# Optimization experiments

Measured on AMD Instinct MI355X. Metric: run time of the kernel, lower is better.

The kernel has to match this reference:

```python
import jax, jax.numpy as jnp
import numpy as np
import math

D_MODEL = 1024
NUM_HEADS = 16
D_HEAD = D_MODEL // NUM_HEADS          # 64
N_FREQ = D_HEAD // 2 + 1               # 33 rfft bins
COMPRESSION_RATIO = 0.5


def setup_inputs() -> dict:
    key = jax.random.key(0)
    k_x, k_qkv, k_out, k_b, k_m = jax.random.split(key, 5)
    B, S = 2, 2048
    x = jax.random.normal(k_x, (B, S, D_MODEL), dtype=jnp.float32)
    # Linear weights stored as [in, out] (torch Linear uses [out, in]; math identical).
    w_qkv = jax.random.normal(k_qkv, (D_MODEL, 3 * D_MODEL), dtype=jnp.float32) / math.sqrt(D_MODEL)
    w_out = jax.random.normal(k_out, (D_MODEL, D_MODEL), dtype=jnp.float32) / math.sqrt(D_MODEL)
    b_out = jax.random.normal(k_b, (D_MODEL,), dtype=jnp.float32) * 0.01
    # Learned per-frequency-bin mask logits of AdaptiveFrequencyMask(d_state=d_head).
    # Initialized around logit(compression_ratio) with small noise.
    init_logit = math.log(COMPRESSION_RATIO / (1.0 - COMPRESSION_RATIO))
    mask_logits = init_logit + 0.1 * jax.random.normal(k_m, (N_FREQ,), dtype=jnp.float32)
    return {"x": x, "w_qkv": w_qkv, "w_out": w_out, "b_out": b_out, "mask_logits": mask_logits}


def _spectral_filter(t, mask):
    # rfft over d_head dim, apply learned soft mask, inverse rfft.  t: [B,H,S,dh]
    tf = jnp.fft.rfft(t, axis=-1)          # [B,H,S,N_FREQ] complex
    tf = tf * mask                          # broadcast real mask over bins
    return jnp.fft.irfft(tf, n=t.shape[-1], axis=-1).astype(t.dtype)


def reference(x, w_qkv, w_out, b_out, mask_logits):
    B, S, D = x.shape
    H, dh = NUM_HEADS, D_HEAD
    qkv = x @ w_qkv                                         # [B,S,3D]
    q, k, v = jnp.split(qkv, 3, axis=-1)
    # [B,S,D] -> [B,H,S,dh]
    to_heads = lambda t: t.reshape(B, S, H, dh).transpose(0, 2, 1, 3)
    q, k, v = to_heads(q), to_heads(k), to_heads(v)
    mask = jax.nn.sigmoid(mask_logits)                      # [N_FREQ]
    q = _spectral_filter(q, mask)
    k = _spectral_filter(k, mask)
    scores = jnp.einsum('bhqd,bhkd->bhqk', q, k) / math.sqrt(dh)
    attn = jax.nn.softmax(scores, axis=-1)                  # dropout p=0 (eval)
    out = jnp.einsum('bhqk,bhkd->bhqd', attn, v)
    out = out.transpose(0, 2, 1, 3).reshape(B, S, D)
    return out @ w_out + b_out
```

## Files before the change

kernel.cpp:

```cpp
#include <hip/hip_runtime.h>

#define S_LEN 2048
#define NH    16
#define DH    64
#define DM    1024
#define NQKV  3072

typedef __attribute__((ext_vector_type(8))) __bf16 bf16x8;
typedef __attribute__((ext_vector_type(4))) float  f32x4;
typedef unsigned short ushort_t;

static __device__ __forceinline__ unsigned short bf16b(float f) {
  return __builtin_bit_cast(unsigned short, (__bf16)f);
}

static __device__ __forceinline__ float exp2v(float x) {
  return __builtin_amdgcn_exp2f(x);
}

static __device__ __forceinline__ bf16x8 pack8(float4 f0, float4 f1) {
  uint4 v;
  v.x = ((unsigned)bf16b(f0.y) << 16) | bf16b(f0.x);
  v.y = ((unsigned)bf16b(f0.w) << 16) | bf16b(f0.z);
  v.z = ((unsigned)bf16b(f1.y) << 16) | bf16b(f1.x);
  v.w = ((unsigned)bf16b(f1.w) << 16) | bf16b(f1.z);
  return __builtin_bit_cast(bf16x8, v);
}

static __device__ __forceinline__ void glds16(const void* g, void* l) {
  __builtin_amdgcn_global_load_lds((const __attribute__((address_space(1))) unsigned int*)g,
                                   (__attribute__((address_space(3))) unsigned int*)l, 16, 0, 0);
}

#define OFF_WT  65536ull
#define OFF_WOT 6356992ull
#define OFF_Q   8454144ull
#define OFF_K   16842752ull
#define OFF_V   25231360ull
#define OFF_AO  33619968ull

__global__ __launch_bounds__(256) void k_prep(const float* __restrict__ wqkv,
                                              const float* __restrict__ wout,
                                              const float* __restrict__ x,
                                              const float* __restrict__ logits,
                                              unsigned short* __restrict__ Wt,
                                              unsigned short* __restrict__ Wot,
                                              unsigned short* __restrict__ xb) {
  __shared__ __align__(16) char sbuf[16640];
  int bid = blockIdx.x;
  int t = threadIdx.x;

  if (bid < 256) {
    float* msk = (float*)sbuf;
    float* Kd  = (float*)(sbuf + 144);
    ushort_t (*Fb)[72] = (ushort_t(*)[72])(sbuf + 416);
    if (t < 33) msk[t] = 1.0f / (1.0f + __expf(-logits[t]));
    __syncthreads();
    if (t < 64) {
      float acc = msk[0];
      #pragma unroll
      for (int f = 1; f < 32; ++f) {
        int r = (f * t) & 63;
        acc += 2.0f * msk[f] * __cosf((float)r * (6.28318530717958647692f / 64.0f));
      }
      acc += msk[32] * ((t & 1) ? -1.0f : 1.0f);
      Kd[t] = acc * (1.0f / 64.0f);
    }
    __syncthreads();
    for (int idx = t; idx < 4096; idx += 256) {
      int j = idx >> 6, i = idx & 63;
      Fb[j][i] = bf16b(Kd[(j - i) & 63]);
    }
    __syncthreads();

    int lane = t & 63, w = t >> 6;
    int m16 = lane & 15, quad = lane >> 4;
    int kx = bid >> 5, yy = bid & 31;
    int which = yy >> 4, h = yy & 15;
    int base = which * 1024 + h * 64;

    bf16x8 af0 = *(const bf16x8*)(&Fb[w * 16 + m16][quad * 8]);
    bf16x8 af1 = *(const bf16x8*)(&Fb[w * 16 + m16][32 + quad * 8]);

    f32x4 acc[8] = {};
    #pragma unroll 2
    for (int n = 0; n < 8; ++n) {
      const float* Wg = wqkv + (size_t)(kx * 128 + n * 16 + m16) * NQKV + base + quad * 8;
      float4 a0 = *(const float4*)(Wg);
      float4 a1 = *(const float4*)(Wg + 4);
      float4 b0 = *(const float4*)(Wg + 32);
      float4 b1 = *(const float4*)(Wg + 36);
      acc[n] = __builtin_amdgcn_mfma_f32_16x16x32_bf16(af0, pack8(a0, a1), acc[n], 0, 0, 0);
      acc[n] = __builtin_amdgcn_mfma_f32_16x16x32_bf16(af1, pack8(b0, b1), acc[n], 0, 0, 0);
    }
    float sc = (which == 0) ? 0.18033688011112042f : 1.0f;
    #pragma unroll
    for (int n = 0; n < 8; ++n) {
      #pragma unroll
      for (int r = 0; r < 4; ++r) {
        int j = w * 16 + quad * 4 + r;
        Wt[(size_t)(base + j) * DM + kx * 128 + n * 16 + m16] = bf16b(acc[n][r] * sc);
      }
    }
  } else if (bid < 768) {
    float (*Ts)[65] = (float(*)[65])sbuf;
    int b1 = bid - 256;
    if (b1 < 256) {
      int kt = b1 & 15, nt = b1 >> 4;
      int cb = 2048 + nt * 64, kbase = kt * 64;
      #pragma unroll
      for (int p = 0; p < 16; ++p) {
        int kk = p * 4 + (t >> 6);
        Ts[kk][t & 63] = wqkv[(size_t)(kbase + kk) * NQKV + cb + (t & 63)];
      }
      __syncthreads();
      #pragma unroll
      for (int p = 0; p < 16; ++p) {
        int nn = p * 4 + (t >> 6);
        Wt[(size_t)(cb + nn) * DM + kbase + (t & 63)] = bf16b(Ts[t & 63][nn]);
      }
    } else {
      int b2 = b1 - 256;
      int kt = b2 & 15, nt = b2 >> 4;
      int cb = nt * 64, kbase = kt * 64;
      #pragma unroll
      for (int p = 0; p < 16; ++p) {
        int kk = p * 4 + (t >> 6);
        Ts[kk][t & 63] = wout[(size_t)(kbase + kk) * DM + cb + (t & 63)];
      }
      __syncthreads();
      #pragma unroll
      for (int p = 0; p < 16; ++p) {
        int nn = p * 4 + (t >> 6);
        Wot[(size_t)(cb + nn) * DM + kbase + (t & 63)] = bf16b(Ts[t & 63][nn]);
      }
    }
  } else {
    size_t i = ((size_t)(bid - 768) * 256 + t) * 8;
    const float4* xp = (const float4*)(x + i);
    float4 a = xp[0], b = xp[1];
    uint4 v;
    v.x = ((unsigned)bf16b(a.y) << 16) | bf16b(a.x);
    v.y = ((unsigned)bf16b(a.w) << 16) | bf16b(a.z);
    v.z = ((unsigned)bf16b(b.y) << 16) | bf16b(b.x);
    v.w = ((unsigned)bf16b(b.w) << 16) | bf16b(b.z);
    *(uint4*)(xb + i) = v;
  }
}

__device__ __forceinline__ void gemm_core_async(const unsigned short* __restrict__ A,
                                                const unsigned short* __restrict__ Bw,
                                                int bm, int bn, unsigned short* smem,
                                                f32x4 (&acc)[4][4]) {
  unsigned short* As = smem;
  unsigned short* Bs = smem + 8192;
  int t = threadIdx.x, lane = t & 63, w = t >> 6;
  int m16 = lane & 15, quad = lane >> 4;
  int wr = (w >> 1) * 64, wc = (w & 1) * 64;
  int lr = lane >> 3, lc = lane & 7;
  int gc = lc ^ lr;
  int xr = m16 & 7;
  const unsigned short* Agb = A  + (size_t)(bm * 128) * DM + gc * 8;
  const unsigned short* Bgb = Bw + (size_t)(bn * 128) * DM + gc * 8;

  for (int k0 = 0; k0 < DM; k0 += 64) {
    #pragma unroll
    for (int p = 0; p < 4; ++p) {
      int row = p * 32 + w * 8 + lr;
      glds16(Agb + (size_t)row * DM + k0, As + row * 64 + lc * 8);
      glds16(Bgb + (size_t)row * DM + k0, Bs + row * 64 + lc * 8);
    }
    __syncthreads();
    #pragma unroll
    for (int kk = 0; kk < 2; ++kk) {
      bf16x8 af[4], bfr[4];
      #pragma unroll
      for (int i = 0; i < 4; ++i)
        af[i] = *(const bf16x8*)(As + (wr + i * 16 + m16) * 64 + ((kk * 4 + quad) ^ xr) * 8);
      #pragma unroll
      for (int j = 0; j < 4; ++j)
        bfr[j] = *(const bf16x8*)(Bs + (wc + j * 16 + m16) * 64 + ((kk * 4 + quad) ^ xr) * 8);
      #pragma unroll
      for (int i = 0; i < 4; ++i)
        #pragma unroll
        for (int j = 0; j < 4; ++j)
          acc[i][j] = __builtin_amdgcn_mfma_f32_16x16x32_bf16(af[i], bfr[j], acc[i][j], 0, 0, 0);
    }
    __syncthreads();
  }
}

__global__ __launch_bounds__(256) void k_gemm_qkv(const unsigned short* __restrict__ xb,
                                                  const unsigned short* __restrict__ Bw,
                                                  unsigned short* __restrict__ Qb,
                                                  unsigned short* __restrict__ Kb,
                                                  unsigned short* __restrict__ Vt) {
  __shared__ __align__(16) unsigned short smem[18432];
  f32x4 acc[4][4] = {};
  int bn = blockIdx.x, bm = blockIdx.y;
  gemm_core_async(xb, Bw, bm, bn, smem, acc);

  int t = threadIdx.x, lane = t & 63, w = t >> 6;
  int m16 = lane & 15, quad = lane >> 4;
  int wr = (w >> 1) * 64, wc = (w & 1) * 64;
  int b = bm >> 4, srow = (bm & 15) * 128;
  int which = bn >> 3;
  ushort_t (*Tr)[130] = (ushort_t(*)[130])smem;
  if (which < 2) {
    #pragma unroll
    for (int i = 0; i < 4; ++i)
      #pragma unroll
      for (int j = 0; j < 4; ++j)
        #pragma unroll
        for (int r = 0; r < 4; ++r)
          Tr[wr + i * 16 + quad * 4 + r][wc + j * 16 + m16] = bf16b(acc[i][j][r]);
    __syncthreads();
    int row = t >> 1, half = t & 1;
    int cloc = bn * 128 + half * 64 - which * 1024;
    int h = cloc >> 6;
    unsigned short* dst = (which ? Kb : Qb) +
        ((size_t)(b * 16 + h) * 2048 + srow + row) * 64;
    #pragma unroll
    for (int p = 0; p < 8; ++p)
      *(uint4*)(dst + p * 8) = *(const uint4*)(&Tr[row][half * 64 + p * 8]);
  } else {
    #pragma unroll
    for (int i = 0; i < 4; ++i)
      #pragma unroll
      for (int j = 0; j < 4; ++j)
        #pragma unroll
        for (int r = 0; r < 4; ++r)
          Tr[wc + j * 16 + m16][wr + i * 16 + quad * 4 + r] = bf16b(acc[i][j][r]);
    __syncthreads();
    int dl = t >> 1, half = t & 1;
    int cloc = (bn - 16) * 128 + dl;
    int h = cloc >> 6, d = cloc & 63;
    unsigned short* dst = Vt + ((size_t)(b * 16 + h) * 64 + d) * 2048 + srow + half * 64;
    #pragma unroll
    for (int p = 0; p < 8; ++p)
      *(uint4*)(dst + p * 8) = *(const uint4*)(&Tr[dl][half * 64 + p * 8]);
  }
}

__global__ __launch_bounds__(512, 4) void k_attn(const unsigned short* __restrict__ Qb,
                                                 const unsigned short* __restrict__ Kb,
                                                 const unsigned short* __restrict__ Vt,
                                                 unsigned short* __restrict__ AO) {
  __shared__ __align__(16) unsigned short smem[25088];
  int t = threadIdx.x;
  int w = t >> 6, lane = t & 63;
  int m16 = lane & 15, quad = lane >> 4;
  int bid = blockIdx.x;
  int jj = bid >> 3;
  int bh = ((jj & 3) << 3) + (bid & 7);
  int qbase = (jj >> 2) * 128 + w * 16;

  const unsigned short* Qp = Qb + ((size_t)bh * S_LEN + qbase + m16) * DH + quad * 8;
  bf16x8 aq0 = *(const bf16x8*)(Qp);
  bf16x8 aq1 = *(const bf16x8*)(Qp + 32);
  const unsigned short* Kbase = Kb + (size_t)bh * S_LEN * DH;
  const unsigned short* Vbase = Vt + (size_t)bh * DH * S_LEN;

  unsigned short* Pw = smem + 16384 + w * 1088;
  int xr = m16 & 7;

  int trow = t >> 3;
  int tcol = t & 7;
  int gswz = tcol ^ (trow & 7);

  f32x4 o[4] = {};
  float l = 0.f;
  f32x4 zero = {0.f, 0.f, 0.f, 0.f};

  glds16(Kbase + (size_t)trow * 64 + gswz * 8,    smem + trow * 64 + tcol * 8);
  glds16(Vbase + (size_t)trow * S_LEN + gswz * 8, smem + 8192 + trow * 64 + tcol * 8);
  __syncthreads();

  #pragma unroll 1
  for (int kt = 0; kt < S_LEN / 64; ++kt) {
    int cur = kt & 1, nxt = cur ^ 1;
    if (kt + 1 < S_LEN / 64) {
      int kk = (kt + 1) * 64;
      glds16(Kbase + (size_t)(kk + trow) * 64 + gswz * 8,
             smem + nxt * 4096 + trow * 64 + tcol * 8);
      glds16(Vbase + (size_t)trow * S_LEN + kk + gswz * 8,
             smem + 8192 + nxt * 4096 + trow * 64 + tcol * 8);
    }
    unsigned short* Ksh = smem + cur * 4096;
    unsigned short* Vsh = smem + 8192 + cur * 4096;

    f32x4 st[4];
    #pragma unroll
    for (int g = 0; g < 4; ++g) {
      int rk = g * 16 + m16;
      bf16x8 kf0 = *(const bf16x8*)(Ksh + rk * 64 + ((quad ^ xr) * 8));
      bf16x8 kf1 = *(const bf16x8*)(Ksh + rk * 64 + (((4 + quad) ^ xr) * 8));
      st[g] = __builtin_amdgcn_mfma_f32_16x16x32_bf16(kf0, aq0, zero, 0, 0, 0);
      st[g] = __builtin_amdgcn_mfma_f32_16x16x32_bf16(kf1, aq1, st[g], 0, 0, 0);
    }
    #pragma unroll
    for (int g = 0; g < 4; ++g) {
      float p0 = exp2v(st[g][0]), p1 = exp2v(st[g][1]);
      float p2 = exp2v(st[g][2]), p3 = exp2v(st[g][3]);
      l += (p0 + p1) + (p2 + p3);
      uint2 pk;
      pk.x = ((unsigned)bf16b(p1) << 16) | bf16b(p0);
      pk.y = ((unsigned)bf16b(p3) << 16) | bf16b(p2);
      *(uint2*)(Pw + m16 * 68 + g * 16 + quad * 4) = pk;
    }
    #pragma unroll
    for (int c = 0; c < 2; ++c) {
      bf16x8 ap = *(const bf16x8*)(Pw + m16 * 68 + c * 32 + quad * 8);
      #pragma unroll
      for (int j = 0; j < 4; ++j) {
        int dv = j * 16 + m16;
        bf16x8 bv = *(const bf16x8*)(Vsh + dv * 64 + (((c * 4 + quad) ^ xr) * 8));
        o[j] = __builtin_amdgcn_mfma_f32_16x16x32_bf16(ap, bv, o[j], 0, 0, 0);
      }
    }
    __syncthreads();
  }

  l += __shfl_xor(l, 16); l += __shfl_xor(l, 32);
  float iv = 1.0f / l;
  int b = bh >> 4, h = bh & 15;
  #pragma unroll
  for (int r = 0; r < 4; ++r) {
    float v0 = __shfl(iv, quad * 4 + r);
    size_t row0 = (size_t)b * S_LEN + qbase + quad * 4 + r;
    unsigned short* d0 = AO + row0 * DM + h * DH + m16;
    #pragma unroll
    for (int j = 0; j < 4; ++j)
      d0[j * 16] = bf16b(o[j][r] * v0);
  }
}

__global__ __launch_bounds__(256) void k_gemm_out(const unsigned short* __restrict__ A,
                                                  const unsigned short* __restrict__ Bw,
                                                  const float* __restrict__ bias,
                                                  float* __restrict__ out) {
  __shared__ __align__(16) unsigned short smem[18432];
  f32x4 acc[4][4] = {};
  int bn = blockIdx.x, bm = blockIdx.y;
  gemm_core_async(A, Bw, bm, bn, smem, acc);

  int t = threadIdx.x, lane = t & 63, w = t >> 6;
  int m16 = lane & 15, quad = lane >> 4;
  int wr = (w >> 1) * 64, wc = (w & 1) * 64;
  #pragma unroll
  for (int i = 0; i < 4; ++i) {
    int grow = bm * 128 + wr + i * 16 + quad * 4;
    #pragma unroll
    for (int j = 0; j < 4; ++j) {
      int gc = bn * 128 + wc + j * 16 + m16;
      float bb = bias[gc];
      #pragma unroll
      for (int r = 0; r < 4; ++r)
        out[(size_t)(grow + r) * DM + gc] = acc[i][j][r] + bb;
    }
  }
}

extern "C" void kernel_launch(void* const* d_in, const int* in_sizes, int n_in,
                              void* d_out, int out_size, void* d_ws, size_t ws_size,
                              hipStream_t stream) {
  const float* x    = (const float*)d_in[0];
  const float* wqkv = (const float*)d_in[1];
  const float* wout = (const float*)d_in[2];
  const float* bout = (const float*)d_in[3];
  const float* mlog = (const float*)d_in[4];
  char* ws = (char*)d_ws;
  unsigned short* Wt  = (unsigned short*)(ws + OFF_WT);
  unsigned short* Wot = (unsigned short*)(ws + OFF_WOT);
  unsigned short* Qb  = (unsigned short*)(ws + OFF_Q);
  unsigned short* Kb  = (unsigned short*)(ws + OFF_K);
  unsigned short* Vt  = (unsigned short*)(ws + OFF_V);
  unsigned short* xb  = (unsigned short*)(ws + OFF_AO);
  unsigned short* AO  = (unsigned short*)(ws + OFF_AO);
  float* out = (float*)d_out;

  k_prep<<<dim3(2816), dim3(256), 0, stream>>>(wqkv, wout, x, mlog, Wt, Wot, xb);
  k_gemm_qkv<<<dim3(24, 32), dim3(256), 0, stream>>>(xb, Wt, Qb, Kb, Vt);
  k_attn<<<dim3(512), dim3(512), 0, stream>>>(Qb, Kb, Vt, AO);
  k_gemm_out<<<dim3(8, 32), dim3(256), 0, stream>>>(AO, Wot, bout, out);
}
```

Baseline: 215.8 us.

## Split attention over two key halves with atomic fp32 accumulation and normalize pass

Splits each head's key range into two halves so the attention grid doubles to 1024 blocks of 256 threads. Each wave now processes 32 query rows, and V is read straight from global memory into registers instead of being staged through LDS. Unnormalized partial outputs and row sums are combined with atomicAdd into zeroed fp32 buffers, and a new k_norm kernel divides and converts to bf16. This is meant to raise parallelism and reuse of each K fragment, at the cost of two memsets, many global atomics and an extra pass over a 16 MB buffer.

```diff
diff --git a/kernel.cpp b/kernel.cpp
--- a/kernel.cpp
+++ b/kernel.cpp
@@ -33,6 +33,7 @@
 }
 
 #define OFF_WT  65536ull
+#define OFF_LB  65536ull
 #define OFF_WOT 6356992ull
 #define OFF_Q   8454144ull
 #define OFF_K   16842752ull
@@ -242,97 +243,146 @@
   }
 }
 
-__global__ __launch_bounds__(512, 4) void k_attn(const unsigned short* __restrict__ Qb,
+__global__ __launch_bounds__(256, 4) void k_attn(const unsigned short* __restrict__ Qb,
                                                  const unsigned short* __restrict__ Kb,
                                                  const unsigned short* __restrict__ Vt,
-                                                 unsigned short* __restrict__ AO) {
-  __shared__ __align__(16) unsigned short smem[25088];
+                                                 float* __restrict__ dout,
+                                                 float* __restrict__ l_buf) {
+  __shared__ __align__(16) unsigned short smem[16896];
   int t = threadIdx.x;
   int w = t >> 6, lane = t & 63;
   int m16 = lane & 15, quad = lane >> 4;
   int bid = blockIdx.x;
-  int jj = bid >> 3;
-  int bh = ((jj & 3) << 3) + (bid & 7);
-  int qbase = (jj >> 2) * 128 + w * 16;
+  int bh = (((bid >> 3) & 3) << 3) + (bid & 7);
+  int rest = bid >> 5;
+  int ks = rest & 1, qtile = rest >> 1;
+  int qbase = qtile * 128 + w * 32;
+  int kbase0 = ks * 1024;
 
   const unsigned short* Qp = Qb + ((size_t)bh * S_LEN + qbase + m16) * DH + quad * 8;
-  bf16x8 aq0 = *(const bf16x8*)(Qp);
-  bf16x8 aq1 = *(const bf16x8*)(Qp + 32);
-  const unsigned short* Kbase = Kb + (size_t)bh * S_LEN * DH;
-  const unsigned short* Vbase = Vt + (size_t)bh * DH * S_LEN;
-
-  unsigned short* Pw = smem + 16384 + w * 1088;
+  bf16x8 aq00 = *(const bf16x8*)(Qp);
+  bf16x8 aq01 = *(const bf16x8*)(Qp + 32);
+  bf16x8 aq10 = *(const bf16x8*)(Qp + 16 * DH);
+  bf16x8 aq11 = *(const bf16x8*)(Qp + 16 * DH + 32);
+  const unsigned short* Kbase = Kb + (size_t)bh * S_LEN * DH + (size_t)kbase0 * DH;
+  const unsigned short* Vbase = Vt + (size_t)bh * DH * S_LEN + kbase0;
+
+  unsigned short* Pw = smem + 8192 + w * 2176;
   int xr = m16 & 7;
 
   int trow = t >> 3;
   int tcol = t & 7;
   int gswz = tcol ^ (trow & 7);
 
-  f32x4 o[4] = {};
-  float l = 0.f;
+  f32x4 o0[4] = {}, o1[4] = {};
+  float l0 = 0.f, l1 = 0.f;
   f32x4 zero = {0.f, 0.f, 0.f, 0.f};
 
-  glds16(Kbase + (size_t)trow * 64 + gswz * 8,    smem + trow * 64 + tcol * 8);
-  glds16(Vbase + (size_t)trow * S_LEN + gswz * 8, smem + 8192 + trow * 64 + tcol * 8);
+  glds16(Kbase + (size_t)trow * 64 + gswz * 8,        smem + trow * 64 + tcol * 8);
+  glds16(Kbase + (size_t)(trow + 32) * 64 + gswz * 8, smem + (trow + 32) * 64 + tcol * 8);
   __syncthreads();
 
   #pragma unroll 1
-  for (int kt = 0; kt < S_LEN / 64; ++kt) {
+  for (int kt = 0; kt < 16; ++kt) {
     int cur = kt & 1, nxt = cur ^ 1;
-    if (kt + 1 < S_LEN / 64) {
-      int kk = (kt + 1) * 64;
+    int k0 = kt * 64;
+    bf16x8 vf[2][4];
+    #pragma unroll
+    for (int c = 0; c < 2; ++c)
+      #pragma unroll
+      for (int j = 0; j < 4; ++j)
+        vf[c][j] = *(const bf16x8*)(Vbase + (size_t)(j * 16 + m16) * S_LEN + k0 + c * 32 + quad * 8);
+    if (kt < 15) {
+      int kk = k0 + 64;
       glds16(Kbase + (size_t)(kk + trow) * 64 + gswz * 8,
              smem + nxt * 4096 + trow * 64 + tcol * 8);
-      glds16(Vbase + (size_t)trow * S_LEN + kk + gswz * 8,
-             smem + 8192 + nxt * 4096 + trow * 64 + tcol * 8);
+      glds16(Kbase + (size_t)(kk + trow + 32) * 64 + gswz * 8,
+             smem + nxt * 4096 + (trow + 32) * 64 + tcol * 8);
     }
     unsigned short* Ksh = smem + cur * 4096;
-    unsigned short* Vsh = smem + 8192 + cur * 4096;
-
-    f32x4 st[4];
+
+    f32x4 st0[4], st1[4];
     #pragma unroll
     for (int g = 0; g < 4; ++g) {
       int rk = g * 16 + m16;
       bf16x8 kf0 = *(const bf16x8*)(Ksh + rk * 64 + ((quad ^ xr) * 8));
       bf16x8 kf1 = *(const bf16x8*)(Ksh + rk * 64 + (((4 + quad) ^ xr) * 8));
-      st[g] = __builtin_amdgcn_mfma_f32_16x16x32_bf16(kf0, aq0, zero, 0, 0, 0);
-      st[g] = __builtin_amdgcn_mfma_f32_16x16x32_bf16(kf1, aq1, st[g], 0, 0, 0);
+      st0[g] = __builtin_amdgcn_mfma_f32_16x16x32_bf16(kf0, aq00, zero, 0, 0, 0);
+      st0[g] = __builtin_amdgcn_mfma_f32_16x16x32_bf16(kf1, aq01, st0[g], 0, 0, 0);
+      st1[g] = __builtin_amdgcn_mfma_f32_16x16x32_bf16(kf0, aq10, zero, 0, 0, 0);
+      st1[g] = __builtin_amdgcn_mfma_f32_16x16x32_bf16(kf1, aq11, st1[g], 0, 0, 0);
     }
     #pragma unroll
     for (int g = 0; g < 4; ++g) {
-      float p0 = exp2v(st[g][0]), p1 = exp2v(st[g][1]);
-      float p2 = exp2v(st[g][2]), p3 = exp2v(st[g][3]);
-      l += (p0 + p1) + (p2 + p3);
+      float p0 = exp2v(st0[g][0]), p1 = exp2v(st0[g][1]);
+      float p2 = exp2v(st0[g][2]), p3 = exp2v(st0[g][3]);
+      l0 += (p0 + p1) + (p2 + p3);
       uint2 pk;
       pk.x = ((unsigned)bf16b(p1) << 16) | bf16b(p0);
       pk.y = ((unsigned)bf16b(p3) << 16) | bf16b(p2);
       *(uint2*)(Pw + m16 * 68 + g * 16 + quad * 4) = pk;
     }
     #pragma unroll
+    for (int g = 0; g < 4; ++g) {
+      float p0 = exp2v(st1[g][0]), p1 = exp2v(st1[g][1]);
+      float p2 = exp2v(st1[g][2]), p3 = exp2v(st1[g][3]);
+      l1 += (p0 + p1) + (p2 + p3);
+      uint2 pk;
+      pk.x = ((unsigned)bf16b(p1) << 16) | bf16b(p0);
+      pk.y = ((unsigned)bf16b(p3) << 16) | bf16b(p2);
+      *(uint2*)(Pw + (16 + m16) * 68 + g * 16 + quad * 4) = pk;
+    }
+    #pragma unroll
     for (int c = 0; c < 2; ++c) {
-      bf16x8 ap = *(const bf16x8*)(Pw + m16 * 68 + c * 32 + quad * 8);
+      bf16x8 ap0 = *(const bf16x8*)(Pw + m16 * 68 + c * 32 + quad * 8);
+      bf16x8 ap1 = *(const bf16x8*)(Pw + (16 + m16) * 68 + c * 32 + quad * 8);
       #pragma unroll
       for (int j = 0; j < 4; ++j) {
-        int dv = j * 16 + m16;
-        bf16x8 bv = *(const bf16x8*)(Vsh + dv * 64 + (((c * 4 + quad) ^ xr) * 8));
-        o[j] = __builtin_amdgcn_mfma_f32_16x16x32_bf16(ap, bv, o[j], 0, 0, 0);
-      }
-    }
-    __syncthreads();
-  }
-
-  l += __shfl_xor(l, 16); l += __shfl_xor(l, 32);
-  float iv = 1.0f / l;
+        o0[j] = __builtin_amdgcn_mfma_f32_16x16x32_bf16(ap0, vf[c][j], o0[j], 0, 0, 0);
+        o1[j] = __builtin_amdgcn_mfma_f32_16x16x32_bf16(ap1, vf[c][j], o1[j], 0, 0, 0);
+      }
+    }
+    __syncthreads();
+  }
+
+  l0 += __shfl_xor(l0, 16); l0 += __shfl_xor(l0, 32);
+  l1 += __shfl_xor(l1, 16); l1 += __shfl_xor(l1, 32);
   int b = bh >> 4, h = bh & 15;
+  if (quad == 0) {
+    atomicAdd(&l_buf[(size_t)bh * S_LEN + qbase + m16], l0);
+    atomicAdd(&l_buf[(size_t)bh * S_LEN + qbase + 16 + m16], l1);
+  }
   #pragma unroll
   for (int r = 0; r < 4; ++r) {
-    float v0 = __shfl(iv, quad * 4 + r);
     size_t row0 = (size_t)b * S_LEN + qbase + quad * 4 + r;
-    unsigned short* d0 = AO + row0 * DM + h * DH + m16;
-    #pragma unroll
-    for (int j = 0; j < 4; ++j)
-      d0[j * 16] = bf16b(o[j][r] * v0);
-  }
+    float* d0 = dout + row0 * DM + h * DH + m16;
+    float* d1 = d0 + (size_t)16 * DM;
+    #pragma unroll
+    for (int j = 0; j < 4; ++j) {
+      atomicAdd(d0 + j * 16, o0[j][r]);
+      atomicAdd(d1 + j * 16, o1[j][r]);
+    }
+  }
+}
+
+__global__ __launch_bounds__(256) void k_norm(const float* __restrict__ dout,
+                                              const float* __restrict__ l_buf,
+                                              unsigned short* __restrict__ AO) {
+  size_t idx = ((size_t)blockIdx.x * 256 + threadIdx.x) * 8;
+  int row = (int)(idx >> 10);
+  int c = (int)(idx & 1023);
+  int b = row >> 11, q = row & 2047, h = c >> 6;
+  float inv = 1.0f / l_buf[(size_t)(b * 16 + h) * S_LEN + q];
+  const float4* sp = (const float4*)(dout + idx);
+  float4 a = sp[0], bb = sp[1];
+  a.x *= inv; a.y *= inv; a.z *= inv; a.w *= inv;
+  bb.x *= inv; bb.y *= inv; bb.z *= inv; bb.w *= inv;
+  uint4 v;
+  v.x = ((unsigned)bf16b(a.y) << 16) | bf16b(a.x);
+  v.y = ((unsigned)bf16b(a.w) << 16) | bf16b(a.z);
+  v.z = ((unsigned)bf16b(bb.y) << 16) | bf16b(bb.x);
+  v.w = ((unsigned)bf16b(bb.w) << 16) | bf16b(bb.z);
+  *(uint4*)(AO + idx) = v;
 }
 
 __global__ __launch_bounds__(256) void k_gemm_out(const unsigned short* __restrict__ A,
@@ -371,6 +421,7 @@
   const float* mlog = (const float*)d_in[4];
   char* ws = (char*)d_ws;
   unsigned short* Wt  = (unsigned short*)(ws + OFF_WT);
+  float*          Lb  = (float*)(ws + OFF_LB);
   unsigned short* Wot = (unsigned short*)(ws + OFF_WOT);
   unsigned short* Qb  = (unsigned short*)(ws + OFF_Q);
   unsigned short* Kb  = (unsigned short*)(ws + OFF_K);
@@ -381,6 +432,9 @@
 
   k_prep<<<dim3(2816), dim3(256), 0, stream>>>(wqkv, wout, x, mlog, Wt, Wot, xb);
   k_gemm_qkv<<<dim3(24, 32), dim3(256), 0, stream>>>(xb, Wt, Qb, Kb, Vt);
-  k_attn<<<dim3(512), dim3(512), 0, stream>>>(Qb, Kb, Vt, AO);
+  hipMemsetAsync(out, 0, (size_t)4096 * 1024 * 4, stream);
+  hipMemsetAsync(Lb, 0, (size_t)32 * 2048 * 4, stream);
+  k_attn<<<dim3(1024), dim3(256), 0, stream>>>(Qb, Kb, Vt, out, Lb);
+  k_norm<<<dim3(2048), dim3(256), 0, stream>>>(out, Lb, AO);
   k_gemm_out<<<dim3(8, 32), dim3(256), 0, stream>>>(AO, Wot, bout, out);
 }
```

Result: slower. 301.8 us (+39.8%).
